# Kernel optimization log

Measured on AMD Instinct MI355X. Metric: run time of the kernel, lower is better.

Reference implementation:

```python
import jax, jax.numpy as jnp
import numpy as np


def setup_inputs() -> dict:
    key = jax.random.key(0)
    k1, k2 = jax.random.split(key)
    B, C, F, H, W = 2, 19, 4, 256, 384
    inp = jax.random.uniform(k1, (B, C, F, H, W), dtype=jnp.float32)
    target = jax.random.randint(k2, (B, F, H, W), 0, C, dtype=jnp.int64)
    return {"input": inp, "target": target}


def reference(input, target):
    """Multi-class Lovasz-Softmax loss, vectorized over classes.

    input:  [B, C, F, H, W] class probabilities in [0, 1]
    target: [B, F, H, W] integer labels in [0, C)
    (No ignore_index values present in the generated inputs, so the
    valid-pixel filter of the original is a no-op.)
    """
    B, C, F, H, W = input.shape
    # flatten to [N, C] pixels-by-classes, matching permute(0,2,3,4,1).view(-1,C)
    probs = jnp.transpose(input, (0, 2, 3, 4, 1)).reshape(-1, C)
    labels = target.reshape(-1)  # [N]

    fg = (labels[:, None] == jnp.arange(C)[None, :]).astype(probs.dtype)  # [N, C]
    errors = jnp.abs(fg - probs)  # [N, C]

    # descending sort per class column (one batched sort instead of C kernels)
    perm = jnp.argsort(-errors, axis=0)  # [N, C]
    errors_sorted = jnp.take_along_axis(errors, perm, axis=0)
    fg_sorted = jnp.take_along_axis(fg, perm, axis=0)

    # Lovasz gradient (Alg. 1), per class
    gts = jnp.sum(fg, axis=0)  # [C]
    intersection = gts[None, :] - jnp.cumsum(fg_sorted, axis=0)
    union = gts[None, :] + jnp.cumsum(1.0 - fg_sorted, axis=0)
    jaccard = 1.0 - intersection / union
    grad = jnp.concatenate([jaccard[:1], jaccard[1:] - jaccard[:-1]], axis=0)

    per_class_loss = jnp.sum(errors_sorted * grad, axis=0)  # [C]

    # mean over classes that are present (fg.sum() > 0), like the loop's `continue`
    present = gts > 0
    n_present = jnp.maximum(jnp.sum(present.astype(probs.dtype)), 1.0)
    return jnp.sum(jnp.where(present, per_class_loss, 0.0)) / n_present
```

## Files before the change

### kernel.cpp

```cpp
#include <hip/hip_runtime.h>


#define NCLS   19
#define FHW    393216
#define NPIX   786432
#define NB     1024
#define PIXPB  8192
#define NCHUNK (NPIX / PIXPB)
#define BPT    (NB / 256)

#define GH_WORDS (NCLS * NB)

typedef float vfloat4 __attribute__((ext_vector_type(4)));

__device__ __forceinline__ void accum_one(unsigned int* h, float p, int lab, int c) {
    const bool fg = (lab == c);
    const float e = fg ? (1.0f - p) : p;
    unsigned int bits = __float_as_uint(1.0f + e);
    unsigned int bkt = (bits - 0x3F800000u) >> 13;
    bkt = min(bkt, (unsigned int)(NB - 1));
    atomicAdd(&h[bkt], 1u + ((unsigned int)fg << 20));
}

__global__ __launch_bounds__(256) void zero_kernel(unsigned int* __restrict__ gH,
                                                   unsigned int* __restrict__ acc) {
    const int i = blockIdx.x * 256 + threadIdx.x;
    gH[i] = 0u;
    if (i < 4) acc[i] = 0u;
}

__global__ __launch_bounds__(256) void hist_kernel(
        const float* __restrict__ input, const int* __restrict__ target,
        unsigned int* __restrict__ gH) {
    __shared__ unsigned int h[NB];
    const int tid = threadIdx.x;
    const int chunk = blockIdx.x;
    const int c = blockIdx.y;

    #pragma unroll
    for (int i = tid; i < NB; i += 256) h[i] = 0u;
    __syncthreads();

    const int pix0 = chunk * PIXPB;
    const int b = pix0 / FHW;
    const int fhw0 = pix0 % FHW;
    const vfloat4* __restrict__ p4 =
        (const vfloat4*)(input + ((long long)(b * NCLS + c)) * FHW + fhw0);
    const int4* __restrict__ l4 = (const int4*)(target + pix0);

    #pragma unroll 8
    for (int i = tid; i < PIXPB / 4; i += 256) {
        vfloat4 p = __builtin_nontemporal_load(&p4[i]);
        int4 l = l4[i];
        accum_one(h, p.x, l.x, c);
        accum_one(h, p.y, l.y, c);
        accum_one(h, p.z, l.z, c);
        accum_one(h, p.w, l.w, c);
    }
    __syncthreads();

    unsigned int* __restrict__ g = gH + c * NB;
    const int rot = (chunk & 15) * 64;
    #pragma unroll
    for (int i = tid; i < NB; i += 256) {
        const int idx = (i + rot) & (NB - 1);
        const unsigned int v = h[idx];
        if (v) atomicAdd(&g[idx], v);
    }
}

__global__ __launch_bounds__(256) void scan_kernel(
        const unsigned int* __restrict__ gH, unsigned int* __restrict__ acc,
        float* __restrict__ out) {
    const int c = blockIdx.x;
    const int tid = threadIdx.x;
    const unsigned int* __restrict__ g = gH + c * NB;

    unsigned int w[BPT];
    const int base = NB - BPT * (tid + 1);
    unsigned int sumN = 0, sumG = 0;
    #pragma unroll
    for (int j = 0; j < BPT; ++j) {
        w[j] = g[base + j];
        sumN += w[j] & 0xFFFFFu;
        sumG += w[j] >> 20;
    }

    __shared__ unsigned long long sd[256];
    const unsigned long long mine = ((unsigned long long)sumG << 32) | sumN;
    sd[tid] = mine;
    __syncthreads();
    for (int off = 1; off < 256; off <<= 1) {
        unsigned long long add = (tid >= off) ? sd[tid - off] : 0ull;
        __syncthreads();
        sd[tid] += add;
        __syncthreads();
    }
    const unsigned long long incl = sd[tid];
    const unsigned long long tot = sd[255];
    const unsigned long long exc = incl - mine;
    const unsigned int G = (unsigned int)(tot >> 32);

    float accv = 0.0f;
    if (G != 0u) {
        const float Gf = (float)G;
        unsigned int r = (unsigned int)exc;
        unsigned int cf = (unsigned int)(exc >> 32);
        float Jprev = __fdividef((float)r, Gf + (float)r - (float)cf);
        #pragma unroll
        for (int j = BPT - 1; j >= 0; --j) {
            const unsigned int nb = w[j] & 0xFFFFFu;
            const unsigned int gb = w[j] >> 20;
            r += nb; cf += gb;
            if (nb) {
                const float Jnew = __fdividef((float)r, Gf + (float)r - (float)cf);
                const float center = ((float)(base + j) + 0.5f) * (1.0f / (float)NB);
                accv += center * (Jnew - Jprev);
                Jprev = Jnew;
            }
        }
    }

    __shared__ float sf[256];
    sf[tid] = accv;
    __syncthreads();
    for (int off = 128; off > 0; off >>= 1) {
        if (tid < off) sf[tid] += sf[tid + off];
        __syncthreads();
    }
    if (tid == 0) {
        if (G != 0u) {
            atomicAdd((float*)&acc[0], sf[0]);
            atomicAdd(&acc[1], 1u);
        }
        __threadfence();
        const unsigned int t = atomicAdd(&acc[2], 1u);
        if (t == NCLS - 1) {
            const float s = atomicAdd((float*)&acc[0], 0.0f);
            const unsigned int k = atomicAdd(&acc[1], 0u);
            out[0] = s / fmaxf((float)k, 1.0f);
        }
    }
}

extern "C" void kernel_launch(void* const* d_in, const int* in_sizes, int n_in,
                              void* d_out, int out_size, void* d_ws, size_t ws_size,
                              hipStream_t stream) {
    const float* input = (const float*)d_in[0];
    const int* target = (const int*)d_in[1];
    float* out = (float*)d_out;

    unsigned int* ws = (unsigned int*)d_ws;
    unsigned int* gH = ws;
    unsigned int* acc = gH + GH_WORDS;

    zero_kernel<<<GH_WORDS / 256, 256, 0, stream>>>(gH, acc);
    hist_kernel<<<dim3(NCHUNK, NCLS), 256, 0, stream>>>(input, target, gH);
    scan_kernel<<<NCLS, 256, 0, stream>>>(gH, acc, out);
}
```

Before: 105.9 us.

## Fuse histogram and scan kernels via last-block-per-class ticket

Merges the scan kernel into the histogram kernel: each block bumps a per-class ticket after flushing its local histogram, and the last block for a class runs the Jaccard scan and the final reduction. This removes one kernel launch and its inter-kernel gap. It also doubles the pixels per block, which halves the number of global atomic flushes, and drops the nontemporal loads and the flush-address rotation. The cost is fewer blocks for parallelism, possible atomic contention without the rotation, and an extra fence on every block.

```diff
diff --git a/kernel.cpp b/kernel.cpp
--- a/kernel.cpp
+++ b/kernel.cpp
@@ -5,11 +5,12 @@
 #define FHW    393216
 #define NPIX   786432
 #define NB     1024
-#define PIXPB  8192
+#define PIXPB  16384
 #define NCHUNK (NPIX / PIXPB)
 #define BPT    (NB / 256)
 
-#define GH_WORDS (NCLS * NB)
+#define GH_WORDS  (NCLS * NB)
+#define TOT_WORDS (GH_WORDS + NCLS + 4)
 
 typedef float vfloat4 __attribute__((ext_vector_type(4)));
 
@@ -22,20 +23,20 @@
     atomicAdd(&h[bkt], 1u + ((unsigned int)fg << 20));
 }
 
-__global__ __launch_bounds__(256) void zero_kernel(unsigned int* __restrict__ gH,
-                                                   unsigned int* __restrict__ acc) {
+__global__ __launch_bounds__(256) void zero_kernel(unsigned int* __restrict__ ws) {
     const int i = blockIdx.x * 256 + threadIdx.x;
-    gH[i] = 0u;
-    if (i < 4) acc[i] = 0u;
+    if (i < TOT_WORDS) ws[i] = 0u;
 }
 
-__global__ __launch_bounds__(256) void hist_kernel(
+__global__ __launch_bounds__(256) void fused_kernel(
         const float* __restrict__ input, const int* __restrict__ target,
-        unsigned int* __restrict__ gH) {
+        unsigned int* __restrict__ gH, float* __restrict__ out) {
     __shared__ unsigned int h[NB];
     const int tid = threadIdx.x;
     const int chunk = blockIdx.x;
     const int c = blockIdx.y;
+    unsigned int* __restrict__ tick = gH + GH_WORDS;
+    unsigned int* __restrict__ acc  = tick + NCLS;
 
     #pragma unroll
     for (int i = tid; i < NB; i += 256) h[i] = 0u;
@@ -48,9 +49,9 @@
         (const vfloat4*)(input + ((long long)(b * NCLS + c)) * FHW + fhw0);
     const int4* __restrict__ l4 = (const int4*)(target + pix0);
 
-    #pragma unroll 8
+    #pragma unroll 4
     for (int i = tid; i < PIXPB / 4; i += 256) {
-        vfloat4 p = __builtin_nontemporal_load(&p4[i]);
+        vfloat4 p = p4[i];
         int4 l = l4[i];
         accum_one(h, p.x, l.x, c);
         accum_one(h, p.y, l.y, c);
@@ -60,28 +61,27 @@
     __syncthreads();
 
     unsigned int* __restrict__ g = gH + c * NB;
-    const int rot = (chunk & 15) * 64;
     #pragma unroll
     for (int i = tid; i < NB; i += 256) {
-        const int idx = (i + rot) & (NB - 1);
-        const unsigned int v = h[idx];
-        if (v) atomicAdd(&g[idx], v);
+        const unsigned int v = h[i];
+        if (v) atomicAdd(&g[i], v);
     }
-}
+    __threadfence();
+    __syncthreads();
 
-__global__ __launch_bounds__(256) void scan_kernel(
-        const unsigned int* __restrict__ gH, unsigned int* __restrict__ acc,
-        float* __restrict__ out) {
-    const int c = blockIdx.x;
-    const int tid = threadIdx.x;
-    const unsigned int* __restrict__ g = gH + c * NB;
+    __shared__ unsigned int sdone;
+    if (tid == 0) sdone = atomicAdd(&tick[c], 1u);
+    __syncthreads();
+    if (sdone != NCHUNK - 1) return;
+    __threadfence();
 
     unsigned int w[BPT];
     const int base = NB - BPT * (tid + 1);
     unsigned int sumN = 0, sumG = 0;
     #pragma unroll
     for (int j = 0; j < BPT; ++j) {
-        w[j] = g[base + j];
+        w[j] = __hip_atomic_load(&g[base + j], __ATOMIC_RELAXED,
+                                 __HIP_MEMORY_SCOPE_AGENT);
         sumN += w[j] & 0xFFFFFu;
         sumG += w[j] >> 20;
     }
@@ -151,10 +151,7 @@
     float* out = (float*)d_out;
 
     unsigned int* ws = (unsigned int*)d_ws;
-    unsigned int* gH = ws;
-    unsigned int* acc = gH + GH_WORDS;
 
-    zero_kernel<<<GH_WORDS / 256, 256, 0, stream>>>(gH, acc);
-    hist_kernel<<<dim3(NCHUNK, NCLS), 256, 0, stream>>>(input, target, gH);
-    scan_kernel<<<NCLS, 256, 0, stream>>>(gH, acc, out);
+    zero_kernel<<<(TOT_WORDS + 255) / 256, 256, 0, stream>>>(ws);
+    fused_kernel<<<dim3(NCHUNK, NCLS), 256, 0, stream>>>(input, target, ws, out);
 }
```

New measurement: 177.4 us. 67.5% more time.
